# Performance work log

Hardware: AMD Instinct MI355X
Metric: run time of the kernel (lower is better)

The kernel has to match this reference:

```python
import jax, jax.numpy as jnp
import numpy as np

B, N1, N2, F = 8, 256, 256, 128


def setup_inputs() -> dict:
    key = jax.random.key(0)
    ks = jax.random.split(key, 12)
    s = 1.0 / np.sqrt(F)
    return {
        "x1": jax.random.normal(ks[0], (B, N1, F), jnp.float32),
        "x2": jax.random.normal(ks[1], (B, N2, F), jnp.float32),
        "valid_edge": (jax.random.uniform(ks[2], (B, N1, N2)) < 0.2).astype(jnp.float32),
        "W_w": jax.random.uniform(ks[3], (F, F), jnp.float32, -s, s),
        "W_b": jax.random.uniform(ks[4], (F,), jnp.float32, -s, s),
        "M_w": jax.random.uniform(ks[5], (F, F), jnp.float32, -s, s),
        "M_b": jax.random.uniform(ks[6], (F,), jnp.float32, -s, s),
        "gru_wih": jax.random.uniform(ks[7], (3 * F, F), jnp.float32, -s, s),
        "gru_whh": jax.random.uniform(ks[8], (3 * F, F), jnp.float32, -s, s),
        "gru_bih": jax.random.uniform(ks[9], (3 * F,), jnp.float32, -s, s),
        "gru_bhh": jax.random.uniform(ks[10], (3 * F,), jnp.float32, -s, s),
    }


def reference(x1, x2, valid_edge, W_w, W_b, M_w, M_b, gru_wih, gru_whh, gru_bih, gru_bhh):
    # m1 = W(x1)  [B,N1,F]
    m1 = jnp.einsum('bnf,gf->bng', x1, W_w) + W_b
    # Apply M once to x2 (equivalent to M on the repeated 4D tensor), then
    # masked max over neighbors j (N2): max_j( M(x2)[b,j,:] * mask[b,i,j] )
    Mx2 = jnp.einsum('bmf,gf->bmg', x2, M_w) + M_b          # [B,N2,F]
    masked = Mx2[:, None, :, :] * valid_edge[..., None]     # [B,N1,N2,F]
    m2 = jnp.max(masked, axis=2)                            # [B,N1,F]
    x = jax.nn.relu(m1 + m2)                                # GRU input
    # GRUCell(input=x, hidden=x1), torch semantics
    xf = x.reshape(-1, F)
    hf = x1.reshape(-1, F)
    gi = xf @ gru_wih.T + gru_bih                           # [B*N1, 3F]
    gh = hf @ gru_whh.T + gru_bhh
    ir, iz, in_ = jnp.split(gi, 3, axis=-1)
    hr, hz, hn = jnp.split(gh, 3, axis=-1)
    r = jax.nn.sigmoid(ir + hr)
    z = jax.nn.sigmoid(iz + hz)
    n = jnp.tanh(in_ + r * hn)
    h = (1.0 - z) * n + z * hf
    return h.reshape(B, N1, F)
```

## Files before the change

kernel.cpp:

```cpp
#include <hip/hip_runtime.h>


#define FDIM 128
#define N2DIM 256

__global__ __launch_bounds__(128)
void k_lin(const float* __restrict__ x1,
           const float* __restrict__ x2,
           const float* __restrict__ Ww,
           const float* __restrict__ Wb,
           const float* __restrict__ Mw,
           const float* __restrict__ Mb,
           float* __restrict__ m1, float* __restrict__ mx2)
{
  int blk = blockIdx.x;
  int which = blk >> 9;
  int row0 = (blk & 511) << 2;
  const float* X  = which ? x2 : x1;
  const float* W  = which ? Mw : Ww;
  const float* Bv = which ? Mb : Wb;
  float* out = which ? mx2 : m1;

  __shared__ float xs[4][FDIM];
  int tid = threadIdx.x;
#pragma unroll
  for (int r = 0; r < 4; ++r)
    xs[r][tid] = X[(size_t)(row0 + r) * FDIM + tid];
  __syncthreads();

  const float* wrow = W + (size_t)tid * FDIM;
  float acc[4] = {0.f,0.f,0.f,0.f};
  for (int k0 = 0; k0 < FDIM; k0 += 4) {
    float4 wv = *(const float4*)(wrow + k0);
#pragma unroll
    for (int r = 0; r < 4; ++r) {
      float4 xv = *(const float4*)(&xs[r][k0]);
      acc[r] += xv.x * wv.x + xv.y * wv.y + xv.z * wv.z + xv.w * wv.w;
    }
  }
  float bv = Bv[tid];
#pragma unroll
  for (int r = 0; r < 4; ++r)
    out[(size_t)(row0 + r) * FDIM + tid] = acc[r] + bv;
}

__global__ __launch_bounds__(256)
void k_fused(const float* __restrict__ ve,
             const float* __restrict__ mx2,
             const float* __restrict__ m1,
             const float* __restrict__ x1,
             const float* __restrict__ wih,
             const float* __restrict__ whh,
             const float* __restrict__ bih,
             const float* __restrict__ bhh,
             float* __restrict__ out)
{
  int row0 = blockIdx.x << 2;
  int b = row0 >> 8;
  int tid = threadIdx.x;

  __shared__ float x_sh[4][FDIM];
  __shared__ float h_sh[4][FDIM];
  __shared__ float gh_sh[3][4][FDIM];
  __shared__ int idx[4][N2DIM];
  __shared__ int cnt[4];
  __shared__ int nz[4];

  for (int t = tid; t < 4 * FDIM; t += 256)
    h_sh[t >> 7][t & 127] = x1[(size_t)row0 * FDIM + t];
  if (tid < 4) { cnt[tid] = 0; nz[tid] = 0; }
  __syncthreads();

  {
    int r = tid >> 6, l = tid & 63;
    const float* e = ve + (size_t)(row0 + r) * N2DIM;
#pragma unroll
    for (int j0 = 0; j0 < N2DIM; j0 += 64) {
      float v = e[j0 + l];
      if (v != 0.0f) { int p = atomicAdd(&cnt[r], 1); idx[r][p] = j0 + l; }
      else nz[r] = 1;
    }
  }
  __syncthreads();

  {
    int half = tid >> 7, f = tid & 127;
    const float* Mbase = mx2 + (size_t)b * N2DIM * FDIM + f;
#pragma unroll
    for (int rr = 0; rr < 2; ++rr) {
      int r = half + (rr << 1);
      int n = cnt[r];
      const int* ix = idx[r];
      float m2 = nz[r] ? 0.0f : -3.0e38f;
      int i = 0;
      for (; i + 8 <= n; i += 8) {
        float v0 = Mbase[(size_t)ix[i]     * FDIM];
        float v1 = Mbase[(size_t)ix[i + 1] * FDIM];
        float v2 = Mbase[(size_t)ix[i + 2] * FDIM];
        float v3 = Mbase[(size_t)ix[i + 3] * FDIM];
        float v4 = Mbase[(size_t)ix[i + 4] * FDIM];
        float v5 = Mbase[(size_t)ix[i + 5] * FDIM];
        float v6 = Mbase[(size_t)ix[i + 6] * FDIM];
        float v7 = Mbase[(size_t)ix[i + 7] * FDIM];
        m2 = fmaxf(m2, fmaxf(fmaxf(fmaxf(v0, v1), fmaxf(v2, v3)),
                             fmaxf(fmaxf(v4, v5), fmaxf(v6, v7))));
      }
      for (; i < n; ++i)
        m2 = fmaxf(m2, Mbase[(size_t)ix[i] * FDIM]);
      float s = m1[(size_t)(row0 + r) * FDIM + f] + m2;
      x_sh[r][f] = fmaxf(s, 0.0f);
    }
  }
  __syncthreads();

  int f = tid & 127;
  int io = tid >> 7;
  const float* Wm = io ? whh : wih;
  const float (*tile)[FDIM] = io ? h_sh : x_sh;
  const float* w0p = Wm + (size_t)f * FDIM;
  const float* w1p = Wm + (size_t)(128 + f) * FDIM;
  const float* w2p = Wm + (size_t)(256 + f) * FDIM;

  float a0[4], a1[4], a2[4];
#pragma unroll
  for (int r = 0; r < 4; ++r) { a0[r] = 0.f; a1[r] = 0.f; a2[r] = 0.f; }

  for (int k0 = 0; k0 < FDIM; k0 += 4) {
    float4 c0 = *(const float4*)(w0p + k0);
    float4 c1 = *(const float4*)(w1p + k0);
    float4 c2 = *(const float4*)(w2p + k0);
#pragma unroll
    for (int r = 0; r < 4; ++r) {
      float4 tv = *(const float4*)(&tile[r][k0]);
      a0[r] += tv.x * c0.x + tv.y * c0.y + tv.z * c0.z + tv.w * c0.w;
      a1[r] += tv.x * c1.x + tv.y * c1.y + tv.z * c1.z + tv.w * c1.w;
      a2[r] += tv.x * c2.x + tv.y * c2.y + tv.z * c2.z + tv.w * c2.w;
    }
  }

  const float* Bv = io ? bhh : bih;
  float b0 = Bv[f], b1 = Bv[128 + f], b2 = Bv[256 + f];

  if (io) {
#pragma unroll
    for (int r = 0; r < 4; ++r) {
      gh_sh[0][r][f] = a0[r] + b0;
      gh_sh[1][r][f] = a1[r] + b1;
      gh_sh[2][r][f] = a2[r] + b2;
    }
  }
  __syncthreads();
  if (!io) {
#pragma unroll
    for (int r = 0; r < 4; ++r) {
      float ir  = a0[r] + b0, iz = a1[r] + b1, in_ = a2[r] + b2;
      float hr  = gh_sh[0][r][f];
      float hz  = gh_sh[1][r][f];
      float hn  = gh_sh[2][r][f];
      float rg  = 1.f / (1.f + __expf(-(ir + hr)));
      float zg  = 1.f / (1.f + __expf(-(iz + hz)));
      float pre = in_ + rg * hn;
      float e2  = __expf(2.f * pre);
      float nn  = 1.f - 2.f / (e2 + 1.f);
      float h   = (1.f - zg) * nn + zg * h_sh[r][f];
      out[(size_t)(row0 + r) * FDIM + f] = h;
    }
  }
}

extern "C" void kernel_launch(void* const* d_in, const int* in_sizes, int n_in,
                              void* d_out, int out_size, void* d_ws, size_t ws_size,
                              hipStream_t stream) {
  (void)in_sizes; (void)n_in; (void)out_size; (void)ws_size;
  const float* x1  = (const float*)d_in[0];
  const float* x2  = (const float*)d_in[1];
  const float* ve  = (const float*)d_in[2];
  const float* Ww  = (const float*)d_in[3];
  const float* Wb  = (const float*)d_in[4];
  const float* Mw  = (const float*)d_in[5];
  const float* Mb  = (const float*)d_in[6];
  const float* wih = (const float*)d_in[7];
  const float* whh = (const float*)d_in[8];
  const float* bih = (const float*)d_in[9];
  const float* bhh = (const float*)d_in[10];
  float* out = (float*)d_out;

  float* ws  = (float*)d_ws;
  float* m1  = ws;
  float* mx2 = ws + 262144;

  hipLaunchKernelGGL(k_lin,   dim3(1024), dim3(128), 0, stream,
                     x1, x2, Ww, Wb, Mw, Mb, m1, mx2);
  hipLaunchKernelGGL(k_fused, dim3(512),  dim3(256), 0, stream,
                     ve, mx2, m1, x1, wih, whh, bih, bhh, out);
}
```

Before: 117.2 us.

## Process eight rows per block and split GRU matmul by gate

Both kernels now handle 8 rows per block instead of 4, halving the grid and doubling reuse of each weight row loaded from global memory. The fused kernel grows to 512 threads. Its GRU matmul is reorganised: 384 threads each own one gate output column and compute both the input and hidden projections for all 8 rows, storing both to shared memory. A separate pass by all threads then applies the gate nonlinearities. The aim is to cut redundant weight traffic, at the cost of fewer blocks (256 per kernel), about 40 KB of shared memory per block, and 128 threads idle during the GRU matmul.

```diff
diff --git a/kernel.cpp b/kernel.cpp
--- a/kernel.cpp
+++ b/kernel.cpp
@@ -14,37 +14,40 @@
            float* __restrict__ m1, float* __restrict__ mx2)
 {
   int blk = blockIdx.x;
-  int which = blk >> 9;
-  int row0 = (blk & 511) << 2;
+  int which = blk >> 8;
+  int row0 = (blk & 255) << 3;
   const float* X  = which ? x2 : x1;
   const float* W  = which ? Mw : Ww;
   const float* Bv = which ? Mb : Wb;
   float* out = which ? mx2 : m1;
 
-  __shared__ float xs[4][FDIM];
+  __shared__ float xs[8][FDIM];
   int tid = threadIdx.x;
 #pragma unroll
-  for (int r = 0; r < 4; ++r)
+  for (int r = 0; r < 8; ++r)
     xs[r][tid] = X[(size_t)(row0 + r) * FDIM + tid];
   __syncthreads();
 
   const float* wrow = W + (size_t)tid * FDIM;
-  float acc[4] = {0.f,0.f,0.f,0.f};
+  float acc[8];
+#pragma unroll
+  for (int r = 0; r < 8; ++r) acc[r] = 0.f;
+
   for (int k0 = 0; k0 < FDIM; k0 += 4) {
     float4 wv = *(const float4*)(wrow + k0);
 #pragma unroll
-    for (int r = 0; r < 4; ++r) {
+    for (int r = 0; r < 8; ++r) {
       float4 xv = *(const float4*)(&xs[r][k0]);
       acc[r] += xv.x * wv.x + xv.y * wv.y + xv.z * wv.z + xv.w * wv.w;
     }
   }
   float bv = Bv[tid];
 #pragma unroll
-  for (int r = 0; r < 4; ++r)
+  for (int r = 0; r < 8; ++r)
     out[(size_t)(row0 + r) * FDIM + tid] = acc[r] + bv;
 }
 
-__global__ __launch_bounds__(256)
+__global__ __launch_bounds__(512)
 void k_fused(const float* __restrict__ ve,
              const float* __restrict__ mx2,
              const float* __restrict__ m1,
@@ -55,20 +58,21 @@
              const float* __restrict__ bhh,
              float* __restrict__ out)
 {
-  int row0 = blockIdx.x << 2;
+  int row0 = blockIdx.x << 3;
   int b = row0 >> 8;
   int tid = threadIdx.x;
 
-  __shared__ float x_sh[4][FDIM];
-  __shared__ float h_sh[4][FDIM];
-  __shared__ float gh_sh[3][4][FDIM];
-  __shared__ int idx[4][N2DIM];
-  __shared__ int cnt[4];
-  __shared__ int nz[4];
+  __shared__ float x_sh[8][FDIM];
+  __shared__ float h_sh[8][FDIM];
+  __shared__ float si_sh[3][8][FDIM];
+  __shared__ float sh_sh[3][8][FDIM];
+  __shared__ int idx[8][N2DIM];
+  __shared__ int cnt[8];
+  __shared__ int nz[8];
 
-  for (int t = tid; t < 4 * FDIM; t += 256)
+  for (int t = tid; t < 8 * FDIM; t += 512)
     h_sh[t >> 7][t & 127] = x1[(size_t)row0 * FDIM + t];
-  if (tid < 4) { cnt[tid] = 0; nz[tid] = 0; }
+  if (tid < 8) { cnt[tid] = 0; nz[tid] = 0; }
   __syncthreads();
 
   {
@@ -84,11 +88,11 @@
   __syncthreads();
 
   {
-    int half = tid >> 7, f = tid & 127;
+    int q = tid >> 7, f = tid & 127;
     const float* Mbase = mx2 + (size_t)b * N2DIM * FDIM + f;
 #pragma unroll
     for (int rr = 0; rr < 2; ++rr) {
-      int r = half + (rr << 1);
+      int r = q + (rr << 2);
       int n = cnt[r];
       const int* ix = idx[r];
       float m2 = nz[r] ? 0.0f : -3.0e38f;
@@ -113,50 +117,47 @@
   }
   __syncthreads();
 
-  int f = tid & 127;
-  int io = tid >> 7;
-  const float* Wm = io ? whh : wih;
-  const float (*tile)[FDIM] = io ? h_sh : x_sh;
-  const float* w0p = Wm + (size_t)f * FDIM;
-  const float* w1p = Wm + (size_t)(128 + f) * FDIM;
-  const float* w2p = Wm + (size_t)(256 + f) * FDIM;
+  if (tid < 384) {
+    int g = tid >> 7, f = tid & 127;
+    const float* wi = wih + (size_t)(g * 128 + f) * FDIM;
+    const float* wh = whh + (size_t)(g * 128 + f) * FDIM;
 
-  float a0[4], a1[4], a2[4];
+    float ai[8], ah[8];
 #pragma unroll
-  for (int r = 0; r < 4; ++r) { a0[r] = 0.f; a1[r] = 0.f; a2[r] = 0.f; }
+    for (int r = 0; r < 8; ++r) { ai[r] = 0.f; ah[r] = 0.f; }
 
-  for (int k0 = 0; k0 < FDIM; k0 += 4) {
-    float4 c0 = *(const float4*)(w0p + k0);
-    float4 c1 = *(const float4*)(w1p + k0);
-    float4 c2 = *(const float4*)(w2p + k0);
+    for (int k0 = 0; k0 < FDIM; k0 += 4) {
+      float4 wiv = *(const float4*)(wi + k0);
+      float4 whv = *(const float4*)(wh + k0);
 #pragma unroll
-    for (int r = 0; r < 4; ++r) {
-      float4 tv = *(const float4*)(&tile[r][k0]);
-      a0[r] += tv.x * c0.x + tv.y * c0.y + tv.z * c0.z + tv.w * c0.w;
-      a1[r] += tv.x * c1.x + tv.y * c1.y + tv.z * c1.z + tv.w * c1.w;
-      a2[r] += tv.x * c2.x + tv.y * c2.y + tv.z * c2.z + tv.w * c2.w;
+      for (int r = 0; r < 8; ++r) {
+        float4 xv = *(const float4*)(&x_sh[r][k0]);
+        float4 hv = *(const float4*)(&h_sh[r][k0]);
+        ai[r] += xv.x * wiv.x + xv.y * wiv.y + xv.z * wiv.z + xv.w * wiv.w;
+        ah[r] += hv.x * whv.x + hv.y * whv.y + hv.z * whv.z + hv.w * whv.w;
+      }
     }
-  }
-
-  const float* Bv = io ? bhh : bih;
-  float b0 = Bv[f], b1 = Bv[128 + f], b2 = Bv[256 + f];
-
-  if (io) {
+    float bi = bih[g * 128 + f];
+    float bh = bhh[g * 128 + f];
 #pragma unroll
-    for (int r = 0; r < 4; ++r) {
-      gh_sh[0][r][f] = a0[r] + b0;
-      gh_sh[1][r][f] = a1[r] + b1;
-      gh_sh[2][r][f] = a2[r] + b2;
+    for (int r = 0; r < 8; ++r) {
+      si_sh[g][r][f] = ai[r] + bi;
+      sh_sh[g][r][f] = ah[r] + bh;
     }
   }
   __syncthreads();
-  if (!io) {
+
+  {
+    int q = tid >> 7, f = tid & 127;
 #pragma unroll
-    for (int r = 0; r < 4; ++r) {
-      float ir  = a0[r] + b0, iz = a1[r] + b1, in_ = a2[r] + b2;
-      float hr  = gh_sh[0][r][f];
-      float hz  = gh_sh[1][r][f];
-      float hn  = gh_sh[2][r][f];
+    for (int rr = 0; rr < 2; ++rr) {
+      int r = q + (rr << 2);
+      float ir  = si_sh[0][r][f];
+      float iz  = si_sh[1][r][f];
+      float in_ = si_sh[2][r][f];
+      float hr  = sh_sh[0][r][f];
+      float hz  = sh_sh[1][r][f];
+      float hn  = sh_sh[2][r][f];
       float rg  = 1.f / (1.f + __expf(-(ir + hr)));
       float zg  = 1.f / (1.f + __expf(-(iz + hz)));
       float pre = in_ + rg * hn;
@@ -189,8 +190,8 @@
   float* m1  = ws;
   float* mx2 = ws + 262144;
 
-  hipLaunchKernelGGL(k_lin,   dim3(1024), dim3(128), 0, stream,
+  hipLaunchKernelGGL(k_lin,   dim3(512), dim3(128), 0, stream,
                      x1, x2, Ww, Wb, Mw, Mb, m1, mx2);
-  hipLaunchKernelGGL(k_fused, dim3(512),  dim3(256), 0, stream,
+  hipLaunchKernelGGL(k_fused, dim3(256), dim3(512), 0, stream,
                      ve, mx2, m1, x1, wih, whh, bih, bhh, out);
 }
```

After: 117.6 us. No clear change (+0.4%).
